# Performance work log

Hardware: AMD Instinct MI355X
Metric: run time of the kernel (lower is better)

The kernel has to match this reference:

```python
import jax, jax.numpy as jnp
import numpy as np

NUM_EMBEDDINGS = 8192
EMBED_DIM = 256
BETA = 0.25  # commitment loss weight (self.beta in the torch module)


def setup_inputs() -> dict:
    key = jax.random.key(0)
    k1, k2 = jax.random.split(key)
    z = jax.random.normal(k1, (16, EMBED_DIM, 32, 32), dtype=jnp.float32)
    # learned codebook (nn.Embedding weight), default init ~ N(0,1); scale for realism
    codebook = jax.random.normal(k2, (NUM_EMBEDDINGS, EMBED_DIM), dtype=jnp.float32)
    return {"z": z, "codebook": codebook}


def reference(z, codebook):
    # channel_last: [B, C, H, W] -> [B, H, W, C]
    zl = jnp.transpose(z, (0, 2, 3, 1))
    # d = ||e||^2 - 2 z.e  (the ||z||^2 term is constant w.r.t. argmin, as in source)
    d = jnp.sum(codebook * codebook, axis=1) - 2.0 * jnp.einsum('bhwd,nd->bhwn', zl, codebook)
    index = jnp.argmin(d, axis=-1)          # [B, H, W] int
    z_q = codebook[index]                   # [B, H, W, C]
    loss = (jnp.mean((jax.lax.stop_gradient(z_q) - zl) ** 2)
            + BETA * jnp.mean((z_q - jax.lax.stop_gradient(zl)) ** 2))
    # straight-through estimator
    z_q_st = zl + jax.lax.stop_gradient(z_q - zl)
    # diversity: mean over batch of (#unique codes used per sample) / (#positions per sample)
    B = index.shape[0]
    flat = index.reshape(B, -1)             # [B, HW]
    presence = jnp.zeros((B, NUM_EMBEDDINGS), jnp.float32).at[
        jnp.arange(B)[:, None], flat].set(1.0)
    diversity = presence.sum() / jnp.float32(flat.size)
    # channel_first: [B, H, W, C] -> [B, C, H, W]
    z_q_out = jnp.transpose(z_q_st, (0, 3, 1, 2))
    return z_q_out, index, loss, diversity
```

## Files before the change

kernel.cpp:

```cpp
#include <hip/hip_runtime.h>
#include <cstdint>

typedef unsigned short u16;
typedef unsigned int   u32;
typedef __attribute__((ext_vector_type(8))) short bf16x8;
typedef __attribute__((ext_vector_type(4))) float f32x4;

#define NPOS    16384
#define DIM     256
#define NCODES  8192
#define ZSTRIDE 262144
#define NELEM   4194304
#define TAU     6e-3f
#define RCH     32


#define WS_AHI    0u
#define WS_ALO    8388608u
#define WS_BHI    16777216u
#define WS_BLO    20971520u
#define WS_E2     25165824u
#define WS_WV1    25198592u
#define WS_WI1    25722880u
#define WS_WV2    26247168u
#define WS_IDX    26771456u
#define WS_PRES   26836992u
#define WS_RCNT   26853376u
#define WS_LDEL   26853380u
#define WS_RLIST  26853632u
#define WS_PART   26919168u
#define WS_RBV    26920448u
#define WS_RBI    29017600u

__device__ __forceinline__ u16 f2bf(float x) {
    u32 u = __float_as_uint(x);
    return (u16)((u + 0x7FFFu + ((u >> 16) & 1u)) >> 16);
}
__device__ __forceinline__ float bf2f(u16 h) { return __uint_as_float((u32)h << 16); }

__device__ __forceinline__ void gload_lds16(const void* g, void* l) {
    __builtin_amdgcn_global_load_lds(
        (const __attribute__((address_space(1))) void*)g,
        (__attribute__((address_space(3))) void*)l, 16, 0, 0);
}

__device__ __forceinline__ void top2_push(float& v1, int& i1, float& v2, float d, int c) {
    const bool better = d < v1;
    v2 = fminf(v2, fmaxf(d, v1));
    v1 = fminf(v1, d);
    if (better) i1 = c;
}
__device__ __forceinline__ void top2_merge(float& v1, int& i1, float& v2,
                                           float ov1, int oi1, float ov2) {
    const bool better = ov1 < v1;
    v2 = fminf(fminf(v2, ov2), fmaxf(v1, ov1));
    v1 = fminf(v1, ov1);
    if (better) i1 = oi1;
}

__global__ __launch_bounds__(256)
void preprocess(const float* __restrict__ cb, const float* __restrict__ z,
                u16* __restrict__ Bhi, u16* __restrict__ Blo,
                u16* __restrict__ Ahi, u16* __restrict__ Alo,
                float* __restrict__ e2, u32* __restrict__ presence,
                int* __restrict__ rcnt, float* __restrict__ ldel) {
    __shared__ u16 his[128 * 34], los[128 * 34];
    const int bid = blockIdx.x;
    const int t   = threadIdx.x;

    if (bid < 2048) {
        if (bid < 16) presence[bid * 256 + t] = 0u;
        if (bid == 16 && t == 0) { rcnt[0] = 0; ldel[0] = 0.0f; }

        const int row  = bid * 4 + (t >> 6);
        const int lane = t & 63;
        const float4 v = *(const float4*)(cb + (size_t)row * DIM + lane * 4);
        float s = v.x * v.x + v.y * v.y + v.z * v.z + v.w * v.w;
#pragma unroll
        for (int o = 32; o > 0; o >>= 1) s += __shfl_xor(s, o);
        if (lane == 0) e2[row] = s;

        const float vv[4] = {v.x, v.y, v.z, v.w};
        u16 h[4], l[4];
#pragma unroll
        for (int j = 0; j < 4; ++j) { h[j] = f2bf(vv[j]); l[j] = f2bf(vv[j] - bf2f(h[j])); }

        const int nt = row >> 7, pr = row & 127, kt = lane >> 3;
        const int q  = (lane & 7) >> 1, off = (lane & 1) * 4;
        const int sw = (pr >> 1) & 3;
        const size_t dst = ((size_t)(nt * 8 + kt) * 128 + pr) * 32 + ((q ^ sw) << 3) + off;
        *(uint2*)(Bhi + dst) = make_uint2((u32)h[0] | ((u32)h[1] << 16), (u32)h[2] | ((u32)h[3] << 16));
        *(uint2*)(Blo + dst) = make_uint2((u32)l[0] | ((u32)l[1] << 16), (u32)l[2] | ((u32)l[3] << 16));
        return;
    }

    const int zb = bid - 2048;
    const int m = zb >> 3, kt = zb & 7;
    const int b = m >> 3, hw0 = (m & 7) * 128;
    const int p = t & 127, ch = t >> 7;

#pragma unroll
    for (int sub = 0; sub < 16; ++sub) {
        const int cl = sub * 2 + ch;
        const float v = z[(size_t)b * ZSTRIDE + (size_t)(kt * 32 + cl) * 1024 + hw0 + p];
        const u16 h = f2bf(v);
        his[p * 34 + cl] = h;
        los[p * 34 + cl] = f2bf(v - bf2f(h));
    }
    __syncthreads();
    const int p2 = t >> 1, c0 = (t & 1) * 2;
    const int sw = (p2 >> 1) & 3;
    const size_t base = ((size_t)(m * 8 + kt) * 128 + p2) * 32;
    u32 wh[8], wl[8];
    const int half = c0 * 8;
#pragma unroll
    for (int j = 0; j < 8; ++j) {
        wh[j] = (u32)his[p2 * 34 + half + 2 * j] | ((u32)his[p2 * 34 + half + 2 * j + 1] << 16);
        wl[j] = (u32)los[p2 * 34 + half + 2 * j] | ((u32)los[p2 * 34 + half + 2 * j + 1] << 16);
    }
    *(uint4*)(Ahi + base + (((c0 + 0) ^ sw) << 3)) = make_uint4(wh[0], wh[1], wh[2], wh[3]);
    *(uint4*)(Ahi + base + (((c0 + 1) ^ sw) << 3)) = make_uint4(wh[4], wh[5], wh[6], wh[7]);
    *(uint4*)(Alo + base + (((c0 + 0) ^ sw) << 3)) = make_uint4(wl[0], wl[1], wl[2], wl[3]);
    *(uint4*)(Alo + base + (((c0 + 1) ^ sw) << 3)) = make_uint4(wl[4], wl[5], wl[6], wl[7]);
}

__global__ __launch_bounds__(256, 2)
void gemm_argmin(const u16* __restrict__ Ahi, const u16* __restrict__ Alo,
                 const u16* __restrict__ Bhi, const u16* __restrict__ Blo,
                 const float* __restrict__ e2,
                 float* __restrict__ wv1, int* __restrict__ wi1, float* __restrict__ wv2) {
    __shared__ u16 sbuf[2][4][4096];
    __shared__ __align__(16) float e2s[1024];
    __shared__ float lv1[256]; __shared__ int li1[256]; __shared__ float lv2[256];

    const int bid = blockIdx.x;
    const int ng  = bid & 7;
    const int mt  = bid >> 3;

    const int tid  = threadIdx.x;
    const int lane = tid & 63;
    const int wvi  = tid >> 6;
    const int wr   = wvi >> 1, wc = wvi & 1;
    const int l15  = lane & 15, lq = lane >> 4;
    const int woff = (tid & 192) * 16;
    const int src  = tid * 8;
    const int sel  = (l15 >> 1) & 3;
    const int ka   = ((lq ^ sel) << 3);

#define FRAG(base, row) (*(const bf16x8*)((base) + (row) * 32 + ka))
#define STAGE(bq, ss_) do {                                                     \
        const int nt_ = ng * 8 + ((ss_) >> 3), kt_ = (ss_) & 7;                 \
        const u16* Ah_ = Ahi + (size_t)(mt * 8 + kt_) * 4096;                   \
        const u16* Al_ = Alo + (size_t)(mt * 8 + kt_) * 4096;                   \
        const u16* Bh_ = Bhi + (size_t)(nt_ * 8 + kt_) * 4096;                  \
        const u16* Bl_ = Blo + (size_t)(nt_ * 8 + kt_) * 4096;                  \
        gload_lds16(Ah_ + src,        (char*)&sbuf[bq][0][0] + woff);           \
        gload_lds16(Ah_ + 2048 + src, (char*)&sbuf[bq][0][0] + 4096 + woff);    \
        gload_lds16(Al_ + src,        (char*)&sbuf[bq][1][0] + woff);           \
        gload_lds16(Al_ + 2048 + src, (char*)&sbuf[bq][1][0] + 4096 + woff);    \
        gload_lds16(Bh_ + src,        (char*)&sbuf[bq][2][0] + woff);           \
        gload_lds16(Bh_ + 2048 + src, (char*)&sbuf[bq][2][0] + 4096 + woff);    \
        gload_lds16(Bl_ + src,        (char*)&sbuf[bq][3][0] + woff);           \
        gload_lds16(Bl_ + 2048 + src, (char*)&sbuf[bq][3][0] + 4096 + woff);    \
    } while (0)

    float rv1[16], rv2[16]; int ri1[16];
#pragma unroll
    for (int e = 0; e < 16; ++e) { rv1[e] = 3e38f; rv2[e] = 3e38f; ri1[e] = 0; }

    f32x4 acc[4][4] = {};
    float e2v[4];
    int cbase = 0;

    reinterpret_cast<float4*>(e2s)[tid] = ((const float4*)e2)[ng * 256 + tid];
    __syncthreads();
    STAGE(0, 0);

    for (int ss = 0; ss < 64; ++ss) {
        const int cur = ss & 1;
        if (ss < 63) {
            STAGE(cur ^ 1, ss + 1);
            asm volatile("s_waitcnt vmcnt(8)" ::: "memory");
        } else {
            asm volatile("s_waitcnt vmcnt(0)" ::: "memory");
        }
        __builtin_amdgcn_s_barrier();
        __builtin_amdgcn_sched_barrier(0);

        if ((ss & 7) == 0) {
            const int ntl = ss >> 3;
            cbase = (ng * 8 + ntl) * 128 + wc * 64 + l15;
            const int eb = ntl * 128 + wc * 64 + l15;
#pragma unroll
            for (int ni = 0; ni < 4; ++ni) e2v[ni] = e2s[eb + ni * 16];
        }

        const u16* Ah = &sbuf[cur][0][0];
        const u16* Al = &sbuf[cur][1][0];
        const u16* Bh = &sbuf[cur][2][0];
        const u16* Bl = &sbuf[cur][3][0];

        bf16x8 ah[4], bh[4], xx[4];
#pragma unroll
        for (int i = 0; i < 4; ++i) ah[i] = FRAG(Ah, wr * 64 + i * 16 + l15);
#pragma unroll
        for (int i = 0; i < 4; ++i) bh[i] = FRAG(Bh, wc * 64 + i * 16 + l15);
#pragma unroll
        for (int i = 0; i < 4; ++i)
#pragma unroll
            for (int j = 0; j < 4; ++j)
                acc[i][j] = __builtin_amdgcn_mfma_f32_16x16x32_bf16(ah[i], bh[j], acc[i][j], 0, 0, 0);
#pragma unroll
        for (int i = 0; i < 4; ++i) xx[i] = FRAG(Bl, wc * 64 + i * 16 + l15);
#pragma unroll
        for (int i = 0; i < 4; ++i)
#pragma unroll
            for (int j = 0; j < 4; ++j)
                acc[i][j] = __builtin_amdgcn_mfma_f32_16x16x32_bf16(ah[i], xx[j], acc[i][j], 0, 0, 0);
#pragma unroll
        for (int i = 0; i < 4; ++i) xx[i] = FRAG(Al, wr * 64 + i * 16 + l15);
#pragma unroll
        for (int i = 0; i < 4; ++i)
#pragma unroll
            for (int j = 0; j < 4; ++j)
                acc[i][j] = __builtin_amdgcn_mfma_f32_16x16x32_bf16(xx[i], bh[j], acc[i][j], 0, 0, 0);

        if ((ss & 7) == 7) {
#pragma unroll
            for (int mi = 0; mi < 4; ++mi)
#pragma unroll
                for (int j = 0; j < 4; ++j) {
                    const int e = mi * 4 + j;
#pragma unroll
                    for (int ni = 0; ni < 4; ++ni) {
                        const float d = fmaf(-2.0f, acc[mi][ni][j], e2v[ni]);
                        top2_push(rv1[e], ri1[e], rv2[e], d, cbase + ni * 16);
                    }
                }
#pragma unroll
            for (int mi = 0; mi < 4; ++mi)
#pragma unroll
                for (int ni = 0; ni < 4; ++ni)
                    acc[mi][ni] = f32x4{0.f, 0.f, 0.f, 0.f};
        }
        __builtin_amdgcn_s_barrier();
    }

#pragma unroll
    for (int mi = 0; mi < 4; ++mi)
#pragma unroll
        for (int j = 0; j < 4; ++j) {
            const int e = mi * 4 + j;
            float v1 = rv1[e], v2 = rv2[e]; int i1 = ri1[e];
#pragma unroll
            for (int off = 1; off <= 8; off <<= 1) {
                const float ov1 = __shfl_xor(v1, off);
                const int   oi1 = __shfl_xor(i1, off);
                const float ov2 = __shfl_xor(v2, off);
                top2_merge(v1, i1, v2, ov1, oi1, ov2);
            }
            if (l15 == 0) {
                const int row = wr * 64 + mi * 16 + lq * 4 + j;
                lv1[row * 2 + wc] = v1; li1[row * 2 + wc] = i1; lv2[row * 2 + wc] = v2;
            }
        }
    __syncthreads();
    if (tid < 128) {
        float v1 = lv1[tid * 2], v2 = lv2[tid * 2]; int i1 = li1[tid * 2];
        top2_merge(v1, i1, v2, lv1[tid * 2 + 1], li1[tid * 2 + 1], lv2[tid * 2 + 1]);
        const size_t o = (size_t)ng * NPOS + (size_t)mt * 128 + tid;
        wv1[o] = v1; wi1[o] = i1; wv2[o] = v2;
    }
#undef FRAG
#undef STAGE
}

__global__ __launch_bounds__(256)
void merge_output(const float* __restrict__ wv1, const int* __restrict__ wi1,
                  const float* __restrict__ wv2,
                  const float* __restrict__ z, const float* __restrict__ cb,
                  float* __restrict__ out, float* __restrict__ out_idxf,
                  float* __restrict__ partial, u32* __restrict__ presence,
                  int* __restrict__ rcnt, int* __restrict__ rlist,
                  int* __restrict__ ws_idx) {
    __shared__ int codes[64];
    __shared__ float red[256];
    const int tile = blockIdx.x;
    const int b    = tile >> 4;
    const int hw0  = (tile & 15) * 64;
    const int tid  = threadIdx.x;
    const int m    = tid & 63;
    const int cg   = tid >> 6;

    if (cg == 0) {
        const int pos = tile * 64 + m;
        float v1 = 3e38f, v2 = 3e38f; int i1 = 0;
#pragma unroll
        for (int g = 0; g < 8; ++g) {
            const size_t o = (size_t)g * NPOS + pos;
            top2_merge(v1, i1, v2, wv1[o], wi1[o], wv2[o]);
        }
        codes[m]      = i1;
        ws_idx[pos]   = i1;
        out_idxf[pos] = (float)i1;
        if (v2 - v1 < TAU) {
            const int s = atomicAdd(rcnt, 1);
            rlist[s] = pos;
        } else {
            atomicOr(&presence[b * 256 + (i1 >> 5)], 1u << (i1 & 31));
        }
    }
    __syncthreads();

    const int code = codes[m];
    const float* crow = cb  + (size_t)code * DIM;
    const float* zb   = z   + (size_t)b * ZSTRIDE + hw0 + m;
    float*       ob   = out + (size_t)b * ZSTRIDE + hw0 + m;

    float lsum = 0.0f;
#pragma unroll
    for (int q = 0; q < 16; ++q) {
        const int c = (cg * 16 + q) * 4;
        const float4 e = *(const float4*)(crow + c);
        const float z0 = zb[(size_t)(c + 0) * 1024];
        const float z1 = zb[(size_t)(c + 1) * 1024];
        const float z2 = zb[(size_t)(c + 2) * 1024];
        const float z3 = zb[(size_t)(c + 3) * 1024];
        const float d0 = e.x - z0, d1 = e.y - z1, d2 = e.z - z2, d3 = e.w - z3;
        lsum += d0 * d0 + d1 * d1 + d2 * d2 + d3 * d3;
        ob[(size_t)(c + 0) * 1024] = z0 + d0;
        ob[(size_t)(c + 1) * 1024] = z1 + d1;
        ob[(size_t)(c + 2) * 1024] = z2 + d2;
        ob[(size_t)(c + 3) * 1024] = z3 + d3;
    }
    red[tid] = lsum;
    __syncthreads();
    for (int o = 128; o > 0; o >>= 1) {
        if (tid < o) red[tid] += red[tid + o];
        __syncthreads();
    }
    if (tid == 0) partial[tile] = red[0];
}

__global__ __launch_bounds__(256)
void rescue_scan(const float* __restrict__ z, const float* __restrict__ cb,
                 const float* __restrict__ e2, const int* __restrict__ rcnt,
                 const int* __restrict__ rlist,
                 float* __restrict__ rbv, int* __restrict__ rbi) {
    __shared__ float zvec[256];
    const int n = rcnt[0];
    const int t = threadIdx.x;
    const int w = t >> 6, l = t & 63;
    const int njobs = n * 8;
    for (int idx = blockIdx.x; idx < njobs; idx += gridDim.x) {
        const int e  = idx >> 3;
        const int cg = idx & 7;
        const int pos = rlist[e];
        const int b = pos >> 10, hw = pos & 1023;
        __syncthreads();
        zvec[t] = z[(size_t)b * ZSTRIDE + (size_t)t * 1024 + hw];
        __syncthreads();

        const int ch = cg * 4 + w;
        const int c0 = ch * 256 + l * 4;
        float bv = 3e38f; int bi = 0x7fffffff;
#pragma unroll
        for (int j = 0; j < 4; ++j) {
            const int c = c0 + j;
            const float* cr = cb + (size_t)c * DIM;
            float a0 = 0.f, a1 = 0.f, a2 = 0.f, a3 = 0.f;
#pragma unroll
            for (int k = 0; k < DIM; k += 16) {
                const float4 v0 = *(const float4*)(cr + k);
                const float4 v1 = *(const float4*)(cr + k + 4);
                const float4 v2 = *(const float4*)(cr + k + 8);
                const float4 v3 = *(const float4*)(cr + k + 12);
                a0 = fmaf(zvec[k + 0], v0.x, a0); a0 = fmaf(zvec[k + 1], v0.y, a0);
                a0 = fmaf(zvec[k + 2], v0.z, a0); a0 = fmaf(zvec[k + 3], v0.w, a0);
                a1 = fmaf(zvec[k + 4], v1.x, a1); a1 = fmaf(zvec[k + 5], v1.y, a1);
                a1 = fmaf(zvec[k + 6], v1.z, a1); a1 = fmaf(zvec[k + 7], v1.w, a1);
                a2 = fmaf(zvec[k + 8], v2.x, a2); a2 = fmaf(zvec[k + 9], v2.y, a2);
                a2 = fmaf(zvec[k +10], v2.z, a2); a2 = fmaf(zvec[k +11], v2.w, a2);
                a3 = fmaf(zvec[k +12], v3.x, a3); a3 = fmaf(zvec[k +13], v3.y, a3);
                a3 = fmaf(zvec[k +14], v3.z, a3); a3 = fmaf(zvec[k +15], v3.w, a3);
            }
            const float dot = (a0 + a1) + (a2 + a3);
            const float d = fmaf(-2.f, dot, e2[c]);
            if (d < bv) { bv = d; bi = c; }
        }
#pragma unroll
        for (int off = 1; off <= 32; off <<= 1) {
            const float ov = __shfl_xor(bv, off);
            const int   oi = __shfl_xor(bi, off);
            if (ov < bv || (ov == bv && oi < bi)) { bv = ov; bi = oi; }
        }
        if (l == 0) { rbv[e * RCH + ch] = bv; rbi[e * RCH + ch] = bi; }
    }
}

__global__ __launch_bounds__(256)
void rescue_fix(const float* __restrict__ z, const float* __restrict__ cb,
                const int* __restrict__ rcnt, const int* __restrict__ rlist,
                const float* __restrict__ rbv, const int* __restrict__ rbi,
                const int* __restrict__ ws_idx,
                float* __restrict__ out_idxf, u32* __restrict__ presence,
                float* __restrict__ out, float* __restrict__ ldel) {
    __shared__ int   bestc_sh;
    __shared__ float red[4];
    const int n = rcnt[0];
    const int t = threadIdx.x;
    for (int e = blockIdx.x; e < n; e += gridDim.x) {
        const int pos = rlist[e];
        const int b = pos >> 10, hw = pos & 1023;
        if (t < 64) {
            float v = 3e38f; int i = 0x7fffffff;
            if (t < 32) { v = rbv[e * RCH + t]; i = rbi[e * RCH + t]; }
#pragma unroll
            for (int off = 1; off <= 32; off <<= 1) {
                const float ov = __shfl_xor(v, off);
                const int   oi = __shfl_xor(i, off);
                if (ov < v || (ov == v && oi < i)) { v = ov; i = oi; }
            }
            if (t == 0) {
                bestc_sh = i;
                out_idxf[pos] = (float)i;
                atomicOr(&presence[b * 256 + (i >> 5)], 1u << (i & 31));
            }
        }
        __syncthreads();
        const int best = bestc_sh;
        const int old  = ws_idx[pos];
        if (best != old) {
            const float zv = z[(size_t)b * ZSTRIDE + (size_t)t * 1024 + hw];
            const float en = cb[(size_t)best * DIM + t];
            const float eo = cb[(size_t)old  * DIM + t];
            const float dn = en - zv, dold = eo - zv;
            out[(size_t)b * ZSTRIDE + (size_t)t * 1024 + hw] = zv + dn;
            float dl = dn * dn - dold * dold;
#pragma unroll
            for (int o = 32; o > 0; o >>= 1) dl += __shfl_xor(dl, o);
            if ((t & 63) == 0) red[t >> 6] = dl;
            __syncthreads();
            if (t == 0) atomicAdd(ldel, red[0] + red[1] + red[2] + red[3]);
        }
        __syncthreads();
    }
}

__global__ __launch_bounds__(256)
void finalize_kernel(const float* __restrict__ partial,
                     const u32* __restrict__ presence,
                     const float* __restrict__ ldel,
                     float* __restrict__ out_loss, float* __restrict__ out_div) {
    __shared__ float sred[256];
    __shared__ int   ired[256];
    const int tid = threadIdx.x;
    float s = partial[tid];
    int cnt = 0;
    for (int w = tid; w < 16 * 256; w += 256) cnt += __popc(presence[w]);
    sred[tid] = s; ired[tid] = cnt;
    __syncthreads();
    for (int o = 128; o > 0; o >>= 1) {
        if (tid < o) { sred[tid] += sred[tid + o]; ired[tid] += ired[tid + o]; }
        __syncthreads();
    }
    if (tid == 0) {
        out_loss[0] = 1.25f * (sred[0] + ldel[0]) / (float)NELEM;
        out_div[0]  = (float)ired[0] / (float)NPOS;
    }
}

extern "C" void kernel_launch(void* const* d_in, const int* in_sizes, int n_in,
                              void* d_out, int out_size, void* d_ws, size_t ws_size,
                              hipStream_t stream) {
    const float* z  = (const float*)d_in[0];
    const float* cb = (const float*)d_in[1];
    float* out = (float*)d_out;
    char*  ws  = (char*)d_ws;

    u16*   Ahi = (u16*)(ws + WS_AHI);
    u16*   Alo = (u16*)(ws + WS_ALO);
    u16*   Bhi = (u16*)(ws + WS_BHI);
    u16*   Blo = (u16*)(ws + WS_BLO);
    float* e2  = (float*)(ws + WS_E2);
    float* wv1 = (float*)(ws + WS_WV1);
    int*   wi1 = (int*)(ws + WS_WI1);
    float* wv2 = (float*)(ws + WS_WV2);
    int*   ws_idx = (int*)(ws + WS_IDX);
    u32*   presence = (u32*)(ws + WS_PRES);
    int*   rcnt  = (int*)(ws + WS_RCNT);
    float* ldel  = (float*)(ws + WS_LDEL);
    int*   rlist = (int*)(ws + WS_RLIST);
    float* partial = (float*)(ws + WS_PART);
    float* rbv = (float*)(ws + WS_RBV);
    int*   rbi = (int*)(ws + WS_RBI);

    float* out_zq   = out;
    float* out_idxf = out + NELEM;
    float* out_loss = out + NELEM + NPOS;
    float* out_div  = out + NELEM + NPOS + 1;

    preprocess<<<3072, 256, 0, stream>>>(cb, z, Bhi, Blo, Ahi, Alo, e2, presence, rcnt, ldel);
    gemm_argmin<<<1024, 256, 0, stream>>>(Ahi, Alo, Bhi, Blo, e2, wv1, wi1, wv2);
    merge_output<<<NPOS / 64, 256, 0, stream>>>(wv1, wi1, wv2, z, cb, out_zq, out_idxf,
                                                partial, presence, rcnt, rlist, ws_idx);
    rescue_scan<<<2048, 256, 0, stream>>>(z, cb, e2, rcnt, rlist, rbv, rbi);
    rescue_fix<<<512, 256, 0, stream>>>(z, cb, rcnt, rlist, rbv, rbi, ws_idx,
                                        out_idxf, presence, out_zq, ldel);
    finalize_kernel<<<1, 256, 0, stream>>>(partial, presence, ldel, out_loss, out_div);
}
```

Before: 263.6 us.

## Enlarge argmin GEMM tile to 256x256 with 8 waves and per-tile top2 output

Moves the distance GEMM from 128x128 tiles with 4 waves to 256x256 tiles with 8 waves, with each wave covering 128 rows. The preprocess layout of the A and B bf16 hi/lo operands is reorganised to match, and the workspace offsets are enlarged. The aim is more MFMA work per byte staged through LDS, which cuts global and LDS traffic per FLOP. In exchange, the kernel uses about 144KB of LDS, so only one block fits per CU. The per-row top2 is now reduced and written after each 256-code tile, giving 32 partials that merge_output must read instead of 8. The explicit vmcnt pipelining is also replaced by a plain __syncthreads per step, which may weaken the overlap between loads and compute.

```diff
diff --git a/kernel.cpp b/kernel.cpp
--- a/kernel.cpp
+++ b/kernel.cpp
@@ -21,16 +21,16 @@
 #define WS_BLO    20971520u
 #define WS_E2     25165824u
 #define WS_WV1    25198592u
-#define WS_WI1    25722880u
-#define WS_WV2    26247168u
-#define WS_IDX    26771456u
-#define WS_PRES   26836992u
-#define WS_RCNT   26853376u
-#define WS_LDEL   26853380u
-#define WS_RLIST  26853632u
-#define WS_PART   26919168u
-#define WS_RBV    26920448u
-#define WS_RBI    29017600u
+#define WS_WI1    27295744u
+#define WS_WV2    29392896u
+#define WS_IDX    31490048u
+#define WS_PRES   31555584u
+#define WS_RCNT   31571968u
+#define WS_LDEL   31571972u
+#define WS_RLIST  31572224u
+#define WS_PART   31637760u
+#define WS_RBV    31638784u
+#define WS_RBI    33735936u
 
 __device__ __forceinline__ u16 f2bf(float x) {
     u32 u = __float_as_uint(x);
@@ -85,18 +85,19 @@
 #pragma unroll
         for (int j = 0; j < 4; ++j) { h[j] = f2bf(vv[j]); l[j] = f2bf(vv[j] - bf2f(h[j])); }
 
-        const int nt = row >> 7, pr = row & 127, kt = lane >> 3;
+        const int nt = row >> 8, pr = row & 255, kt = lane >> 3;
         const int q  = (lane & 7) >> 1, off = (lane & 1) * 4;
         const int sw = (pr >> 1) & 3;
-        const size_t dst = ((size_t)(nt * 8 + kt) * 128 + pr) * 32 + ((q ^ sw) << 3) + off;
+        const size_t dst = ((size_t)(nt * 8 + kt) * 256 + pr) * 32 + ((q ^ sw) << 3) + off;
         *(uint2*)(Bhi + dst) = make_uint2((u32)h[0] | ((u32)h[1] << 16), (u32)h[2] | ((u32)h[3] << 16));
         *(uint2*)(Blo + dst) = make_uint2((u32)l[0] | ((u32)l[1] << 16), (u32)l[2] | ((u32)l[3] << 16));
         return;
     }
 
     const int zb = bid - 2048;
-    const int m = zb >> 3, kt = zb & 7;
-    const int b = m >> 3, hw0 = (m & 7) * 128;
+    const int m128 = zb >> 3, kt = zb & 7;
+    const int mtb = m128 >> 1, prb = (m128 & 1) * 128;
+    const int b = m128 >> 3, hw0 = (m128 & 7) * 128;
     const int p = t & 127, ch = t >> 7;
 
 #pragma unroll
@@ -110,7 +111,7 @@
     __syncthreads();
     const int p2 = t >> 1, c0 = (t & 1) * 2;
     const int sw = (p2 >> 1) & 3;
-    const size_t base = ((size_t)(m * 8 + kt) * 128 + p2) * 32;
+    const size_t base = ((size_t)(mtb * 8 + kt) * 256 + prb + p2) * 32;
     u32 wh[8], wl[8];
     const int half = c0 * 8;
 #pragma unroll
@@ -124,73 +125,65 @@
     *(uint4*)(Alo + base + (((c0 + 1) ^ sw) << 3)) = make_uint4(wl[4], wl[5], wl[6], wl[7]);
 }
 
-__global__ __launch_bounds__(256, 2)
-void gemm_argmin(const u16* __restrict__ Ahi, const u16* __restrict__ Alo,
-                 const u16* __restrict__ Bhi, const u16* __restrict__ Blo,
-                 const float* __restrict__ e2,
-                 float* __restrict__ wv1, int* __restrict__ wi1, float* __restrict__ wv2) {
-    __shared__ u16 sbuf[2][4][4096];
+__global__ __launch_bounds__(512, 2)
+void gemm256(const u16* __restrict__ Ahi, const u16* __restrict__ Alo,
+             const u16* __restrict__ Bhi, const u16* __restrict__ Blo,
+             const float* __restrict__ e2,
+             float* __restrict__ wv1, int* __restrict__ wi1, float* __restrict__ wv2) {
+    __shared__ u16 sbuf[2][4][8192];
     __shared__ __align__(16) float e2s[1024];
-    __shared__ float lv1[256]; __shared__ int li1[256]; __shared__ float lv2[256];
+    __shared__ float lv1[1024]; __shared__ int li1[1024]; __shared__ float lv2[1024];
 
     const int bid = blockIdx.x;
     const int ng  = bid & 7;
-    const int mt  = bid >> 3;
+    const int mtb = bid >> 3;
 
     const int tid  = threadIdx.x;
     const int lane = tid & 63;
-    const int wvi  = tid >> 6;
-    const int wr   = wvi >> 1, wc = wvi & 1;
+    const int wave = tid >> 6;
+    const int wr   = wave >> 2, wc = wave & 3;
     const int l15  = lane & 15, lq = lane >> 4;
-    const int woff = (tid & 192) * 16;
+    const int woff = wave * 1024;
     const int src  = tid * 8;
     const int sel  = (l15 >> 1) & 3;
     const int ka   = ((lq ^ sel) << 3);
 
 #define FRAG(base, row) (*(const bf16x8*)((base) + (row) * 32 + ka))
 #define STAGE(bq, ss_) do {                                                     \
-        const int nt_ = ng * 8 + ((ss_) >> 3), kt_ = (ss_) & 7;                 \
-        const u16* Ah_ = Ahi + (size_t)(mt * 8 + kt_) * 4096;                   \
-        const u16* Al_ = Alo + (size_t)(mt * 8 + kt_) * 4096;                   \
-        const u16* Bh_ = Bhi + (size_t)(nt_ * 8 + kt_) * 4096;                  \
-        const u16* Bl_ = Blo + (size_t)(nt_ * 8 + kt_) * 4096;                  \
+        const int ntl_ = (ss_) >> 3, kt_ = (ss_) & 7;                           \
+        const int nt_  = ng * 4 + ntl_;                                         \
+        const u16* Ah_ = Ahi + (size_t)(mtb * 8 + kt_) * 8192;                  \
+        const u16* Al_ = Alo + (size_t)(mtb * 8 + kt_) * 8192;                  \
+        const u16* Bh_ = Bhi + (size_t)(nt_ * 8 + kt_) * 8192;                  \
+        const u16* Bl_ = Blo + (size_t)(nt_ * 8 + kt_) * 8192;                  \
         gload_lds16(Ah_ + src,        (char*)&sbuf[bq][0][0] + woff);           \
-        gload_lds16(Ah_ + 2048 + src, (char*)&sbuf[bq][0][0] + 4096 + woff);    \
+        gload_lds16(Ah_ + 4096 + src, (char*)&sbuf[bq][0][0] + 8192 + woff);    \
         gload_lds16(Al_ + src,        (char*)&sbuf[bq][1][0] + woff);           \
-        gload_lds16(Al_ + 2048 + src, (char*)&sbuf[bq][1][0] + 4096 + woff);    \
+        gload_lds16(Al_ + 4096 + src, (char*)&sbuf[bq][1][0] + 8192 + woff);    \
         gload_lds16(Bh_ + src,        (char*)&sbuf[bq][2][0] + woff);           \
-        gload_lds16(Bh_ + 2048 + src, (char*)&sbuf[bq][2][0] + 4096 + woff);    \
+        gload_lds16(Bh_ + 4096 + src, (char*)&sbuf[bq][2][0] + 8192 + woff);    \
         gload_lds16(Bl_ + src,        (char*)&sbuf[bq][3][0] + woff);           \
-        gload_lds16(Bl_ + 2048 + src, (char*)&sbuf[bq][3][0] + 4096 + woff);    \
+        gload_lds16(Bl_ + 4096 + src, (char*)&sbuf[bq][3][0] + 8192 + woff);    \
     } while (0)
 
-    float rv1[16], rv2[16]; int ri1[16];
-#pragma unroll
-    for (int e = 0; e < 16; ++e) { rv1[e] = 3e38f; rv2[e] = 3e38f; ri1[e] = 0; }
-
-    f32x4 acc[4][4] = {};
+    f32x4 acc[8][4] = {};
     float e2v[4];
     int cbase = 0;
 
-    reinterpret_cast<float4*>(e2s)[tid] = ((const float4*)e2)[ng * 256 + tid];
+    e2s[tid]       = e2[ng * 1024 + tid];
+    e2s[tid + 512] = e2[ng * 1024 + 512 + tid];
     __syncthreads();
     STAGE(0, 0);
-
-    for (int ss = 0; ss < 64; ++ss) {
+    __syncthreads();
+
+    for (int ss = 0; ss < 32; ++ss) {
         const int cur = ss & 1;
-        if (ss < 63) {
-            STAGE(cur ^ 1, ss + 1);
-            asm volatile("s_waitcnt vmcnt(8)" ::: "memory");
-        } else {
-            asm volatile("s_waitcnt vmcnt(0)" ::: "memory");
-        }
-        __builtin_amdgcn_s_barrier();
-        __builtin_amdgcn_sched_barrier(0);
+        if (ss < 31) STAGE(cur ^ 1, ss + 1);
 
         if ((ss & 7) == 0) {
             const int ntl = ss >> 3;
-            cbase = (ng * 8 + ntl) * 128 + wc * 64 + l15;
-            const int eb = ntl * 128 + wc * 64 + l15;
+            cbase = (ng * 4 + ntl) * 256 + wc * 64 + l15;
+            const int eb = ntl * 256 + wc * 64 + l15;
 #pragma unroll
             for (int ni = 0; ni < 4; ++ni) e2v[ni] = e2s[eb + ni * 16];
         }
@@ -200,76 +193,71 @@
         const u16* Bh = &sbuf[cur][2][0];
         const u16* Bl = &sbuf[cur][3][0];
 
-        bf16x8 ah[4], bh[4], xx[4];
-#pragma unroll
-        for (int i = 0; i < 4; ++i) ah[i] = FRAG(Ah, wr * 64 + i * 16 + l15);
+        bf16x8 ah[8], bh[4], xx[8];
+#pragma unroll
+        for (int i = 0; i < 8; ++i) ah[i] = FRAG(Ah, wr * 128 + i * 16 + l15);
 #pragma unroll
         for (int i = 0; i < 4; ++i) bh[i] = FRAG(Bh, wc * 64 + i * 16 + l15);
 #pragma unroll
-        for (int i = 0; i < 4; ++i)
+        for (int i = 0; i < 8; ++i)
 #pragma unroll
             for (int j = 0; j < 4; ++j)
                 acc[i][j] = __builtin_amdgcn_mfma_f32_16x16x32_bf16(ah[i], bh[j], acc[i][j], 0, 0, 0);
 #pragma unroll
-        for (int i = 0; i < 4; ++i) xx[i] = FRAG(Bl, wc * 64 + i * 16 + l15);
-#pragma unroll
-        for (int i = 0; i < 4; ++i)
+        for (int j = 0; j < 4; ++j) xx[j] = FRAG(Bl, wc * 64 + j * 16 + l15);
+#pragma unroll
+        for (int i = 0; i < 8; ++i)
 #pragma unroll
             for (int j = 0; j < 4; ++j)
                 acc[i][j] = __builtin_amdgcn_mfma_f32_16x16x32_bf16(ah[i], xx[j], acc[i][j], 0, 0, 0);
 #pragma unroll
-        for (int i = 0; i < 4; ++i) xx[i] = FRAG(Al, wr * 64 + i * 16 + l15);
-#pragma unroll
-        for (int i = 0; i < 4; ++i)
+        for (int i = 0; i < 8; ++i) xx[i] = FRAG(Al, wr * 128 + i * 16 + l15);
+#pragma unroll
+        for (int i = 0; i < 8; ++i)
 #pragma unroll
             for (int j = 0; j < 4; ++j)
                 acc[i][j] = __builtin_amdgcn_mfma_f32_16x16x32_bf16(xx[i], bh[j], acc[i][j], 0, 0, 0);
 
         if ((ss & 7) == 7) {
-#pragma unroll
-            for (int mi = 0; mi < 4; ++mi)
+            const int ntl = ss >> 3;
+#pragma unroll
+            for (int mi = 0; mi < 8; ++mi)
 #pragma unroll
                 for (int j = 0; j < 4; ++j) {
-                    const int e = mi * 4 + j;
+                    float v1 = 3e38f, v2 = 3e38f; int i1 = 0;
 #pragma unroll
                     for (int ni = 0; ni < 4; ++ni) {
                         const float d = fmaf(-2.0f, acc[mi][ni][j], e2v[ni]);
-                        top2_push(rv1[e], ri1[e], rv2[e], d, cbase + ni * 16);
+                        top2_push(v1, i1, v2, d, cbase + ni * 16);
+                    }
+#pragma unroll
+                    for (int off = 1; off <= 8; off <<= 1) {
+                        const float ov1 = __shfl_xor(v1, off);
+                        const int   oi1 = __shfl_xor(i1, off);
+                        const float ov2 = __shfl_xor(v2, off);
+                        top2_merge(v1, i1, v2, ov1, oi1, ov2);
+                    }
+                    if (l15 == 0) {
+                        const int row = wr * 128 + mi * 16 + lq * 4 + j;
+                        lv1[row * 4 + wc] = v1; li1[row * 4 + wc] = i1; lv2[row * 4 + wc] = v2;
                     }
                 }
-#pragma unroll
-            for (int mi = 0; mi < 4; ++mi)
+            __syncthreads();
+            if (tid < 256) {
+                float v1 = lv1[tid * 4], v2 = lv2[tid * 4]; int i1 = li1[tid * 4];
+#pragma unroll
+                for (int g = 1; g < 4; ++g)
+                    top2_merge(v1, i1, v2, lv1[tid * 4 + g], li1[tid * 4 + g], lv2[tid * 4 + g]);
+                const size_t o = (size_t)(ng * 4 + ntl) * NPOS + (size_t)mtb * 256 + tid;
+                wv1[o] = v1; wi1[o] = i1; wv2[o] = v2;
+            }
+#pragma unroll
+            for (int mi = 0; mi < 8; ++mi)
 #pragma unroll
                 for (int ni = 0; ni < 4; ++ni)
                     acc[mi][ni] = f32x4{0.f, 0.f, 0.f, 0.f};
         }
-        __builtin_amdgcn_s_barrier();
-    }
-
-#pragma unroll
-    for (int mi = 0; mi < 4; ++mi)
-#pragma unroll
-        for (int j = 0; j < 4; ++j) {
-            const int e = mi * 4 + j;
-            float v1 = rv1[e], v2 = rv2[e]; int i1 = ri1[e];
-#pragma unroll
-            for (int off = 1; off <= 8; off <<= 1) {
-                const float ov1 = __shfl_xor(v1, off);
-                const int   oi1 = __shfl_xor(i1, off);
-                const float ov2 = __shfl_xor(v2, off);
-                top2_merge(v1, i1, v2, ov1, oi1, ov2);
-            }
-            if (l15 == 0) {
-                const int row = wr * 64 + mi * 16 + lq * 4 + j;
-                lv1[row * 2 + wc] = v1; li1[row * 2 + wc] = i1; lv2[row * 2 + wc] = v2;
-            }
-        }
-    __syncthreads();
-    if (tid < 128) {
-        float v1 = lv1[tid * 2], v2 = lv2[tid * 2]; int i1 = li1[tid * 2];
-        top2_merge(v1, i1, v2, lv1[tid * 2 + 1], li1[tid * 2 + 1], lv2[tid * 2 + 1]);
-        const size_t o = (size_t)ng * NPOS + (size_t)mt * 128 + tid;
-        wv1[o] = v1; wi1[o] = i1; wv2[o] = v2;
+        __syncthreads();
     }
 #undef FRAG
 #undef STAGE
@@ -296,7 +284,7 @@
         const int pos = tile * 64 + m;
         float v1 = 3e38f, v2 = 3e38f; int i1 = 0;
 #pragma unroll
-        for (int g = 0; g < 8; ++g) {
+        for (int g = 0; g < 32; ++g) {
             const size_t o = (size_t)g * NPOS + pos;
             top2_merge(v1, i1, v2, wv1[o], wi1[o], wv2[o]);
         }
@@ -501,7 +489,7 @@
     float* out_div  = out + NELEM + NPOS + 1;
 
     preprocess<<<3072, 256, 0, stream>>>(cb, z, Bhi, Blo, Ahi, Alo, e2, presence, rcnt, ldel);
-    gemm_argmin<<<1024, 256, 0, stream>>>(Ahi, Alo, Bhi, Blo, e2, wv1, wi1, wv2);
+    gemm256<<<512, 512, 0, stream>>>(Ahi, Alo, Bhi, Blo, e2, wv1, wi1, wv2);
     merge_output<<<NPOS / 64, 256, 0, stream>>>(wv1, wi1, wv2, z, cb, out_zq, out_idxf,
                                                 partial, presence, rcnt, rlist, ws_idx);
     rescue_scan<<<2048, 256, 0, stream>>>(z, cb, e2, rcnt, rlist, rbv, rbi);
```

After: 298.3 us. 1.13x slower.

## Single-buffer LDS staging and raise gemm_argmin occupancy to five blocks

Applied to the files above, without the earlier changes.

The GEMM+argmin kernel drops LDS double buffering and uses one 32 KB staging buffer. The per-block codebook-norm cache in LDS goes away: norms are read straight from global memory, and the scratch arrays for the reduction reuse the staging buffer. Launch bounds go from 2 to 5 blocks per CU. The aim is to hide memory latency through more resident waves instead of in-block prefetch. The cost is that loads and MFMA compute no longer overlap within a block, there are extra barriers, and the tighter register cap (about 102 VGPRs) risks spilling the 64-float accumulators and the top-2 state.

```diff
diff --git a/kernel.cpp b/kernel.cpp
--- a/kernel.cpp
+++ b/kernel.cpp
@@ -124,14 +124,12 @@
     *(uint4*)(Alo + base + (((c0 + 1) ^ sw) << 3)) = make_uint4(wl[4], wl[5], wl[6], wl[7]);
 }
 
-__global__ __launch_bounds__(256, 2)
+__global__ __launch_bounds__(256, 5)
 void gemm_argmin(const u16* __restrict__ Ahi, const u16* __restrict__ Alo,
                  const u16* __restrict__ Bhi, const u16* __restrict__ Blo,
                  const float* __restrict__ e2,
                  float* __restrict__ wv1, int* __restrict__ wi1, float* __restrict__ wv2) {
-    __shared__ u16 sbuf[2][4][4096];
-    __shared__ __align__(16) float e2s[1024];
-    __shared__ float lv1[256]; __shared__ int li1[256]; __shared__ float lv2[256];
+    __shared__ u16 sbuf[4][4096];
 
     const int bid = blockIdx.x;
     const int ng  = bid & 7;
@@ -148,20 +146,20 @@
     const int ka   = ((lq ^ sel) << 3);
 
 #define FRAG(base, row) (*(const bf16x8*)((base) + (row) * 32 + ka))
-#define STAGE(bq, ss_) do {                                                     \
+#define STAGE(ss_) do {                                                         \
         const int nt_ = ng * 8 + ((ss_) >> 3), kt_ = (ss_) & 7;                 \
         const u16* Ah_ = Ahi + (size_t)(mt * 8 + kt_) * 4096;                   \
         const u16* Al_ = Alo + (size_t)(mt * 8 + kt_) * 4096;                   \
         const u16* Bh_ = Bhi + (size_t)(nt_ * 8 + kt_) * 4096;                  \
         const u16* Bl_ = Blo + (size_t)(nt_ * 8 + kt_) * 4096;                  \
-        gload_lds16(Ah_ + src,        (char*)&sbuf[bq][0][0] + woff);           \
-        gload_lds16(Ah_ + 2048 + src, (char*)&sbuf[bq][0][0] + 4096 + woff);    \
-        gload_lds16(Al_ + src,        (char*)&sbuf[bq][1][0] + woff);           \
-        gload_lds16(Al_ + 2048 + src, (char*)&sbuf[bq][1][0] + 4096 + woff);    \
-        gload_lds16(Bh_ + src,        (char*)&sbuf[bq][2][0] + woff);           \
-        gload_lds16(Bh_ + 2048 + src, (char*)&sbuf[bq][2][0] + 4096 + woff);    \
-        gload_lds16(Bl_ + src,        (char*)&sbuf[bq][3][0] + woff);           \
-        gload_lds16(Bl_ + 2048 + src, (char*)&sbuf[bq][3][0] + 4096 + woff);    \
+        gload_lds16(Ah_ + src,        (char*)&sbuf[0][0] + woff);               \
+        gload_lds16(Ah_ + 2048 + src, (char*)&sbuf[0][0] + 4096 + woff);        \
+        gload_lds16(Al_ + src,        (char*)&sbuf[1][0] + woff);               \
+        gload_lds16(Al_ + 2048 + src, (char*)&sbuf[1][0] + 4096 + woff);        \
+        gload_lds16(Bh_ + src,        (char*)&sbuf[2][0] + woff);               \
+        gload_lds16(Bh_ + 2048 + src, (char*)&sbuf[2][0] + 4096 + woff);        \
+        gload_lds16(Bl_ + src,        (char*)&sbuf[3][0] + woff);               \
+        gload_lds16(Bl_ + 2048 + src, (char*)&sbuf[3][0] + 4096 + woff);        \
     } while (0)
 
     float rv1[16], rv2[16]; int ri1[16];
@@ -172,33 +170,21 @@
     float e2v[4];
     int cbase = 0;
 
-    reinterpret_cast<float4*>(e2s)[tid] = ((const float4*)e2)[ng * 256 + tid];
+    STAGE(0);
     __syncthreads();
-    STAGE(0, 0);
 
     for (int ss = 0; ss < 64; ++ss) {
-        const int cur = ss & 1;
-        if (ss < 63) {
-            STAGE(cur ^ 1, ss + 1);
-            asm volatile("s_waitcnt vmcnt(8)" ::: "memory");
-        } else {
-            asm volatile("s_waitcnt vmcnt(0)" ::: "memory");
-        }
-        __builtin_amdgcn_s_barrier();
-        __builtin_amdgcn_sched_barrier(0);
-
         if ((ss & 7) == 0) {
-            const int ntl = ss >> 3;
-            cbase = (ng * 8 + ntl) * 128 + wc * 64 + l15;
-            const int eb = ntl * 128 + wc * 64 + l15;
-#pragma unroll
-            for (int ni = 0; ni < 4; ++ni) e2v[ni] = e2s[eb + ni * 16];
-        }
-
-        const u16* Ah = &sbuf[cur][0][0];
-        const u16* Al = &sbuf[cur][1][0];
-        const u16* Bh = &sbuf[cur][2][0];
-        const u16* Bl = &sbuf[cur][3][0];
+            const int nt = ng * 8 + (ss >> 3);
+            cbase = nt * 128 + wc * 64 + l15;
+#pragma unroll
+            for (int ni = 0; ni < 4; ++ni) e2v[ni] = e2[cbase + ni * 16];
+        }
+
+        const u16* Ah = &sbuf[0][0];
+        const u16* Al = &sbuf[1][0];
+        const u16* Bh = &sbuf[2][0];
+        const u16* Bl = &sbuf[3][0];
 
         bf16x8 ah[4], bh[4], xx[4];
 #pragma unroll
@@ -243,8 +229,17 @@
                 for (int ni = 0; ni < 4; ++ni)
                     acc[mi][ni] = f32x4{0.f, 0.f, 0.f, 0.f};
         }
-        __builtin_amdgcn_s_barrier();
-    }
+
+        __syncthreads();
+        if (ss < 63) {
+            STAGE(ss + 1);
+            __syncthreads();
+        }
+    }
+
+    float* lv1 = (float*)&sbuf[0][0];
+    int*   li1 = (int*)((char*)&sbuf[0][0] + 4096);
+    float* lv2 = (float*)((char*)&sbuf[0][0] + 8192);
 
 #pragma unroll
     for (int mi = 0; mi < 4; ++mi)
```

Measured after the change: 557.1 us. 2.11x slower.
